# Kernel tuning notes

Measured on AMD Instinct MI355X. Metric: run time of the kernel, lower is better.

## Reference

```python
import jax, jax.numpy as jnp
import numpy as np

B, D, A = 512, 32, 10
NUM_CODES, CODE_DIM = 512, 64
COMMIT = 0.25


def _conv(x, w, b):
    # NHWC input, HWIO kernel, SAME padding, stride 1 (flax nn.Conv defaults)
    y = jax.lax.conv_general_dilated(x, w, (1, 1), 'SAME',
                                     dimension_numbers=('NHWC', 'HWIO', 'NHWC'))
    return y + b


def setup_inputs() -> dict:
    key = jax.random.key(0)
    ks = jax.random.split(key, 16)
    def rn(k, shape, scale):
        return jax.random.normal(k, shape, dtype=jnp.float32) * scale
    inp = {
        'x': rn(ks[0], (B, D, D), 1.0),
        'conv1_w': rn(ks[1], (3, 3, 1, 32), 0.3),
        'conv1_b': jnp.zeros((32,), jnp.float32),
        'conv2_w': rn(ks[2], (3, 3, 32, 64), 0.06),
        'conv2_b': jnp.zeros((64,), jnp.float32),
        'codebook': rn(ks[3], (NUM_CODES, CODE_DIM), 0.12),  # variance_scaling fan_in-ish
        'w1': rn(ks[4], (D * D * 64, 128), 0.004),
        'b1': jnp.zeros((128,), jnp.float32),
        'w2': rn(ks[5], (128, 128), 0.09),
        'b2': jnp.zeros((128,), jnp.float32),
        'w3': rn(ks[6], (128, 128), 0.09),
        'b3': jnp.zeros((128,), jnp.float32),
        'wa1': rn(ks[7], (128, 128), 0.09),
        'ba1': jnp.zeros((128,), jnp.float32),
        'wa2': rn(ks[8], (128, A), 0.09),
        'ba2': jnp.zeros((A,), jnp.float32),
        'wc1': rn(ks[9], (128, 128), 0.09),
        'bc1': jnp.zeros((128,), jnp.float32),
        'wc2': rn(ks[10], (128, 128), 0.09),
        'bc2': jnp.zeros((128,), jnp.float32),
        'wc3': rn(ks[11], (128, 1), 0.09),
        'bc3': jnp.zeros((1,), jnp.float32),
    }
    return inp


def reference(x, conv1_w, conv1_b, conv2_w, conv2_b, codebook,
              w1, b1, w2, b2, w3, b3,
              wa1, ba1, wa2, ba2,
              wc1, bc1, wc2, bc2, wc3, bc3):
    h = x.reshape(-1, D, D, 1)
    h = jax.nn.relu(_conv(h, conv1_w, conv1_b))
    h = jax.nn.relu(_conv(h, conv2_w, conv2_b))  # [B, D, D, 64]

    # --- Vector quantization (cdist + argmin + gather, straight-through) ---
    flat = h.reshape(-1, CODE_DIM)  # [B*D*D, 64]
    distances = (jnp.sum(flat ** 2, axis=1, keepdims=True)
                 - 2.0 * flat @ codebook.T
                 + jnp.sum(codebook ** 2, axis=1)[None, :])  # [N, num_codes]
    encoding_indices = jnp.argmin(distances, axis=1)
    quantized = codebook[encoding_indices].reshape(h.shape)
    quantized = h + jax.lax.stop_gradient(quantized - h)  # straight-through
    e_latent = jnp.mean((jax.lax.stop_gradient(quantized) - h) ** 2)
    q_latent = jnp.mean((quantized - jax.lax.stop_gradient(h)) ** 2)
    vq_loss = q_latent + COMMIT * e_latent

    # --- MLP trunk + actor-critic heads ---
    emb = quantized.reshape(quantized.shape[0], -1)
    emb = jax.nn.relu(emb @ w1 + b1)
    emb = jax.nn.relu(emb @ w2 + b2)
    emb = jax.nn.relu(emb @ w3 + b3)

    a = jax.nn.relu(emb @ wa1 + ba1)
    probs = jax.nn.softmax(a @ wa2 + ba2, axis=-1)  # Categorical probs

    c = jax.nn.relu(emb @ wc1 + bc1)
    c = jax.nn.relu(c @ wc2 + bc2)
    value = jnp.squeeze(c @ wc3 + bc3, axis=-1)

    return probs, value, vq_loss, encoding_indices
```

## Files before the change

### kernel.cpp

```cpp
#include <hip/hip_runtime.h>
#include <math.h>

#define NB 512
#define DD 32
#define NPX 1024
#define NTOT 524288
#define NC 512
#define CD 64

typedef float v2f __attribute__((ext_vector_type(2)));
typedef _Float16 hf;
typedef hf hf8 __attribute__((ext_vector_type(8)));
typedef float f32x4 __attribute__((ext_vector_type(4)));

__device__ __forceinline__ v2f pkfma(v2f a, v2f b, v2f c) {
    return __builtin_elementwise_fma(a, b, c);
}
__device__ __forceinline__ v2f splat2(float s) { v2f r; r.x = s; r.y = s; return r; }

__device__ __forceinline__ f32x4 mfma16(hf8 a, hf8 b, f32x4 c) {
    return __builtin_amdgcn_mfma_f32_16x16x32_f16(a, b, c, 0, 0, 0);
}

__device__ __forceinline__ float np_sumsq64(const float* a, int stride) {
    float r[8];
    #pragma unroll
    for (int j = 0; j < 8; ++j) {
        float v = a[j * stride];
        r[j] = __fmul_rn(v, v);
    }
    #pragma unroll
    for (int i = 1; i < 8; ++i)
        #pragma unroll
        for (int j = 0; j < 8; ++j) {
            float v = a[(i * 8 + j) * stride];
            r[j] = __fadd_rn(r[j], __fmul_rn(v, v));
        }
    return __fadd_rn(__fadd_rn(__fadd_rn(r[0], r[1]), __fadd_rn(r[2], r[3])),
                     __fadd_rn(__fadd_rn(r[4], r[5]), __fadd_rn(r[6], r[7])));
}

__global__ __launch_bounds__(256) void k_conv1(const float* __restrict__ x,
                                               const float* __restrict__ w,
                                               const float* __restrict__ bias,
                                               float* __restrict__ h1,
                                               const float* __restrict__ cb,
                                               const float* __restrict__ c2w,
                                               float* __restrict__ cnorm,
                                               hf* __restrict__ cbh,
                                               hf* __restrict__ cbl,
                                               hf* __restrict__ wTh,
                                               hf* __restrict__ wTl,
                                               float* __restrict__ accv) {
    const int b = blockIdx.x;
    const int tid = threadIdx.x;
    {
        int t = b * 256 + tid;
        if (t < NC)
            cnorm[t] = np_sumsq64(cb + (size_t)t * CD, 1);
        if (b < 128) {
            float a = cb[t] * 256.f;
            hf h0 = (hf)a;
            float rl = (a - (float)h0) * 2048.f;
            cbh[t] = h0;
            cbl[t] = (hf)rl;
        }
        if (b >= 128 && b < 200) {
            int t2 = (b - 128) * 256 + tid;
            if (t2 < 18432) {
                int s9 = t2 >> 11, rem = t2 & 2047;
                int co = rem >> 5, ci = rem & 31;
                float a = c2w[s9 * 2048 + ci * 64 + co] * 256.f;
                hf h0 = (hf)a;
                float rl = (a - (float)h0) * 2048.f;
                wTh[t2] = h0;
                wTl[t2] = (hf)rl;
            }
        }
        if (t == 0) accv[0] = 0.f;
    }
    __shared__ float xs[34][34];
    for (int i = tid; i < 34 * 34; i += 256) {
        int yy = i / 34, xx = i - yy * 34;
        float v = 0.f;
        if (yy >= 1 && yy <= 32 && xx >= 1 && xx <= 32)
            v = x[(size_t)b * NPX + (yy - 1) * 32 + (xx - 1)];
        xs[yy][xx] = v;
    }
    __syncthreads();
    for (int rep = 0; rep < 4; ++rep) {
        int px = tid + rep * 256;
        int y = px >> 5, xc = px & 31;
        v2f acc2[16];
        #pragma unroll
        for (int c = 0; c < 16; ++c) acc2[c] = splat2(0.f);
        #pragma unroll
        for (int dy = 0; dy < 3; ++dy)
        #pragma unroll
        for (int dx = 0; dx < 3; ++dx) {
            float a = xs[y + dy][xc + dx];
            v2f av = splat2(a);
            const v2f* wr = (const v2f*)(w + (dy * 3 + dx) * 32);
            #pragma unroll
            for (int c = 0; c < 16; ++c) acc2[c] = pkfma(av, wr[c], acc2[c]);
        }
        float4* out = (float4*)(h1 + ((size_t)b * NPX + px) * 32);
        #pragma unroll
        for (int q = 0; q < 8; ++q) {
            float4 v;
            v.x = fmaxf(__fadd_rn(acc2[q*2+0].x, bias[q*4+0]), 0.f);
            v.y = fmaxf(__fadd_rn(acc2[q*2+0].y, bias[q*4+1]), 0.f);
            v.z = fmaxf(__fadd_rn(acc2[q*2+1].x, bias[q*4+2]), 0.f);
            v.w = fmaxf(__fadd_rn(acc2[q*2+1].y, bias[q*4+3]), 0.f);
            out[q] = v;
        }
    }
}

#define CI_P 40
__global__ __launch_bounds__(512, 4) void k_conv2(const float* __restrict__ h1,
                                                  const hf* __restrict__ wTh,
                                                  const hf* __restrict__ wTl,
                                                  const float* __restrict__ bias,
                                                  float* __restrict__ h) {
    __shared__ hf Ah[10 * 34 * CI_P];
    __shared__ hf Al[10 * 34 * CI_P];
    const int blk = blockIdx.x;
    const int b = blk >> 2, strip = blk & 3;
    const int r0 = strip * 8;
    const int tid = threadIdx.x;
    for (int i = tid; i < 640; i += 512) {
        int ci = i & 31, rem = i >> 5;
        int ry = rem >> 1, colx = (rem & 1) * 33;
        int idx = (ry * 34 + colx) * CI_P + ci;
        Ah[idx] = (hf)0.f;
        Al[idx] = (hf)0.f;
    }
    #pragma unroll
    for (int r = 0; r < 5; ++r) {
        int j = tid + r * 512;
        int ci4 = j & 7, xc = (j >> 3) & 31, ry = j >> 8;
        int gy = r0 - 1 + ry;
        float4 v = make_float4(0.f, 0.f, 0.f, 0.f);
        if (gy >= 0 && gy < 32)
            v = *(const float4*)(h1 + ((size_t)b * NPX + gy * 32 + xc) * 32 + ci4 * 4);
        int bi = (ry * 34 + xc + 1) * CI_P + ci4 * 4;
        float fv[4] = {v.x, v.y, v.z, v.w};
        #pragma unroll
        for (int q = 0; q < 4; ++q) {
            float a = fv[q] * 256.f;
            hf h0 = (hf)a;
            float rl = (a - (float)h0) * 2048.f;
            Ah[bi + q] = h0;
            Al[bi + q] = (hf)rl;
        }
    }
    __syncthreads();
    const int w = tid >> 6, l = tid & 63;
    const int i16 = l & 15, j4 = l >> 4;
    #pragma unroll 1
    for (int ntp = 0; ntp < 2; ++ntp) {
        f32x4 hi[2][2], mid[2][2], llt[2][2];
        #pragma unroll
        for (int s = 0; s < 2; ++s)
            #pragma unroll
            for (int n = 0; n < 2; ++n) {
                hi[s][n] = f32x4{0.f, 0.f, 0.f, 0.f};
                mid[s][n] = f32x4{0.f, 0.f, 0.f, 0.f};
                llt[s][n] = f32x4{0.f, 0.f, 0.f, 0.f};
            }
        #pragma unroll 1
        for (int s9 = 0; s9 < 9; ++s9) {
            const int dy = s9 / 3, dx = s9 - dy * 3;
            hf8 a_h[2], a_l[2];
            #pragma unroll
            for (int s = 0; s < 2; ++s) {
                int ofs = ((w + dy) * 34 + (s * 16 + i16 + dx)) * CI_P + 8 * j4;
                a_h[s] = *(const hf8*)(Ah + ofs);
                a_l[s] = *(const hf8*)(Al + ofs);
            }
            #pragma unroll
            for (int ntl = 0; ntl < 2; ++ntl) {
                const int nt = ntp * 2 + ntl;
                const int wofs = (s9 * 64 + nt * 16 + i16) * 32 + 8 * j4;
                const hf8 b_h = *(const hf8*)(wTh + wofs);
                const hf8 b_l = *(const hf8*)(wTl + wofs);
                #pragma unroll
                for (int s = 0; s < 2; ++s) {
                    hi[s][ntl]  = mfma16(a_h[s], b_h, hi[s][ntl]);
                    mid[s][ntl] = mfma16(a_h[s], b_l, mid[s][ntl]);
                    mid[s][ntl] = mfma16(a_l[s], b_h, mid[s][ntl]);
                    llt[s][ntl] = mfma16(a_l[s], b_l, llt[s][ntl]);
                }
            }
        }
        #pragma unroll
        for (int ntl = 0; ntl < 2; ++ntl) {
            const int co = (ntp * 2 + ntl) * 16 + i16;
            const float bco = bias[co];
            #pragma unroll
            for (int s = 0; s < 2; ++s) {
                #pragma unroll
                for (int r = 0; r < 4; ++r) {
                    float comb = fmaf(mid[s][ntl][r], 4.8828125e-4f,
                                 fmaf(llt[s][ntl][r], 2.384185791015625e-7f,
                                      hi[s][ntl][r]));
                    float hv = fmaxf(
                        __fadd_rn(__fmul_rn(comb, 1.52587890625e-5f), bco), 0.f);
                    int px = w * 32 + s * 16 + j4 * 4 + r;
                    h[((size_t)b * NPX + r0 * 32 + px) * 64 + co] = hv;
                }
            }
        }
    }
}

#define TAU 1e-3f
__global__ __launch_bounds__(512, 4) void k_vq(const float* __restrict__ h,
                                               const float* __restrict__ h1,
                                               const float* __restrict__ c2w,
                                               const float* __restrict__ c2b,
                                               const float* __restrict__ cb,
                                               const hf* __restrict__ cbh,
                                               const hf* __restrict__ cbl,
                                               const float* __restrict__ cnorm,
                                               int* __restrict__ idxout,
                                               float* __restrict__ fidx,
                                               float* __restrict__ lossacc) {
    __shared__ float4 Ats[16][256];
    __shared__ float Hs[256];
    __shared__ float cn_lds[512];
    __shared__ int   mis_lds[256];
    __shared__ float r_v[512];
    __shared__ int   r_i[512];
    __shared__ int   rlist[256];
    __shared__ float hex_lds[64];
    __shared__ int   rcnt;
    const int tid = threadIdx.x;
    const size_t base = (size_t)blockIdx.x * 256;
    if (tid == 0) rcnt = 0;
    {
        const int px = tid & 255, half = tid >> 8;
        const float4* src = (const float4*)(h + (base + px) * 64 + half * 32);
        #pragma unroll
        for (int j = 0; j < 8; ++j)
            Ats[half * 8 + j][px] = src[j];
    }
    cn_lds[tid] = cnorm[tid];
    __syncthreads();
    if (tid < 256) {
        float f[64];
        #pragma unroll
        for (int kg = 0; kg < 16; ++kg) {
            float4 v = Ats[kg][tid];
            f[kg*4+0] = v.x; f[kg*4+1] = v.y; f[kg*4+2] = v.z; f[kg*4+3] = v.w;
        }
        float r[8];
        #pragma unroll
        for (int j = 0; j < 8; ++j) r[j] = __fmul_rn(f[j], f[j]);
        #pragma unroll
        for (int i = 1; i < 8; ++i)
            #pragma unroll
            for (int j = 0; j < 8; ++j)
                r[j] = __fadd_rn(r[j], __fmul_rn(f[i*8+j], f[i*8+j]));
        Hs[tid] = __fadd_rn(__fadd_rn(__fadd_rn(r[0], r[1]), __fadd_rn(r[2], r[3])),
                            __fadd_rn(__fadd_rn(r[4], r[5]), __fadd_rn(r[6], r[7])));
    }
    __syncthreads();
    const int w = tid >> 6, l = tid & 63;
    const int co = l & 15, g = l >> 4;
    const int pxw = w * 32;
    hf8 ah[2][2], al[2][2];
    #pragma unroll
    for (int s = 0; s < 2; ++s)
        #pragma unroll
        for (int ks = 0; ks < 2; ++ks) {
            float4 q0 = Ats[ks * 8 + g * 2 + 0][pxw + s * 16 + co];
            float4 q1 = Ats[ks * 8 + g * 2 + 1][pxw + s * 16 + co];
            float fv[8] = {q0.x, q0.y, q0.z, q0.w, q1.x, q1.y, q1.z, q1.w};
            #pragma unroll
            for (int j = 0; j < 8; ++j) {
                float fa = fv[j] * 256.f;
                hf h0 = (hf)fa;
                float rl = (fa - (float)h0) * 2048.f;
                ah[s][ks][j] = h0;
                al[s][ks][j] = (hf)rl;
            }
        }
    float Hr[2][4];
    #pragma unroll
    for (int s = 0; s < 2; ++s)
        #pragma unroll
        for (int r = 0; r < 4; ++r)
            Hr[s][r] = Hs[pxw + s * 16 + g * 4 + r];
    float minv[2][4], min2[2][4];
    int   mini[2][4];
    #pragma unroll
    for (int s = 0; s < 2; ++s)
        #pragma unroll
        for (int r = 0; r < 4; ++r) {
            minv[s][r] = 3.4e38f; min2[s][r] = 3.4e38f; mini[s][r] = 0;
        }
    const hf* pbh = cbh + (size_t)co * 64 + g * 8;
    const hf* pbl = cbl + (size_t)co * 64 + g * 8;
    #pragma unroll 1
    for (int t = 0; t < 32; ++t) {
        const hf8 bh0 = *(const hf8*)(pbh + (size_t)t * 1024);
        const hf8 bh1 = *(const hf8*)(pbh + (size_t)t * 1024 + 32);
        const hf8 bl0 = *(const hf8*)(pbl + (size_t)t * 1024);
        const hf8 bl1 = *(const hf8*)(pbl + (size_t)t * 1024 + 32);
        const float cn = cn_lds[t * 16 + co];
        #pragma unroll
        for (int s = 0; s < 2; ++s) {
            f32x4 hi = {0.f, 0.f, 0.f, 0.f};
            f32x4 lo = {0.f, 0.f, 0.f, 0.f};
            f32x4 ll = {0.f, 0.f, 0.f, 0.f};
            lo = mfma16(ah[s][0], bl0, lo);
            lo = mfma16(al[s][0], bh0, lo);
            ll = mfma16(al[s][0], bl0, ll);
            hi = mfma16(ah[s][0], bh0, hi);
            lo = mfma16(ah[s][1], bl1, lo);
            lo = mfma16(al[s][1], bh1, lo);
            ll = mfma16(al[s][1], bl1, ll);
            hi = mfma16(ah[s][1], bh1, hi);
            #pragma unroll
            for (int r = 0; r < 4; ++r) {
                float comb = fmaf(lo[r], 4.8828125e-4f,
                             fmaf(ll[r], 2.384185791015625e-7f, hi[r]));
                float d = __fadd_rn(__fsub_rn(Hr[s][r],
                              __fmul_rn(3.0517578125e-5f, comb)), cn);
                if (d < minv[s][r]) {
                    min2[s][r] = minv[s][r];
                    minv[s][r] = d; mini[s][r] = t * 16 + co;
                } else if (d < min2[s][r]) {
                    min2[s][r] = d;
                }
            }
        }
    }
    #pragma unroll
    for (int s = 0; s < 2; ++s)
        #pragma unroll
        for (int r = 0; r < 4; ++r) {
            float v1 = minv[s][r], v2 = min2[s][r];
            int i1 = mini[s][r];
            #pragma unroll
            for (int off = 1; off < 16; off <<= 1) {
                float vo  = __shfl_xor(v1, off, 64);
                int   io  = __shfl_xor(i1, off, 64);
                float v2o = __shfl_xor(v2, off, 64);
                if (vo < v1 || (vo == v1 && io < i1)) {
                    v2 = fminf(v1, v2o);
                    v1 = vo; i1 = io;
                } else {
                    v2 = fminf(v2, vo);
                }
            }
            if (co == 0) {
                int pxo = pxw + s * 16 + g * 4 + r;
                mis_lds[pxo] = i1;
                if (v2 - v1 <= TAU) {
                    int slot = atomicAdd(&rcnt, 1);
                    rlist[slot] = pxo;
                }
            }
        }
    __syncthreads();
    const int nresc = rcnt;
    for (int rr = 0; rr < nresc; ++rr) {
        const int px = rlist[rr];
        const int gpx = (int)base + px;
        const int bimg = gpx >> 10, pp = gpx & 1023;
        const int py = pp >> 5, pxx = pp & 31;
        if (tid < 64) {
            float acc = 0.f;
            #pragma unroll 1
            for (int s9 = 0; s9 < 9; ++s9) {
                const int dy = s9 / 3, dx = s9 - dy * 3;
                const int gy = py + dy - 1, gx = pxx + dx - 1;
                if (gy >= 0 && gy < 32 && gx >= 0 && gx < 32) {
                    const float* hp = h1 + ((size_t)bimg * NPX + gy * 32 + gx) * 32;
                    const float* wp = c2w + s9 * 2048 + tid;
                    #pragma unroll
                    for (int ci = 0; ci < 32; ++ci)
                        acc = fmaf(hp[ci], wp[ci * 64], acc);
                }
            }
            hex_lds[tid] = fmaxf(__fadd_rn(acc, c2b[tid]), 0.f);
        }
        __syncthreads();
        const float Hp = np_sumsq64(hex_lds, 1);
        float acc0 = 0.f;
        const float* crow0 = cb + (size_t)tid * 64;
        #pragma unroll
        for (int kg = 0; kg < 16; ++kg) {
            acc0 = fmaf(hex_lds[kg*4+0], crow0[kg*4+0], acc0);
            acc0 = fmaf(hex_lds[kg*4+1], crow0[kg*4+1], acc0);
            acc0 = fmaf(hex_lds[kg*4+2], crow0[kg*4+2], acc0);
            acc0 = fmaf(hex_lds[kg*4+3], crow0[kg*4+3], acc0);
        }
        r_v[tid] = __fadd_rn(__fsub_rn(Hp, __fmul_rn(2.f, acc0)), cn_lds[tid]);
        r_i[tid] = tid;
        __syncthreads();
        for (int st = 256; st > 0; st >>= 1) {
            if (tid < st) {
                float vo = r_v[tid + st]; int io = r_i[tid + st];
                if (vo < r_v[tid] || (vo == r_v[tid] && io < r_i[tid])) {
                    r_v[tid] = vo; r_i[tid] = io;
                }
            }
            __syncthreads();
        }
        if (tid == 0) mis_lds[px] = r_i[0];
        __syncthreads();
    }
    if (tid < 256) {
        int bi = mis_lds[tid];
        idxout[base + tid] = bi;
        fidx[base + tid] = (float)bi;
        float ls = 0.f;
        const float* crow = cb + (size_t)bi * 64;
        #pragma unroll
        for (int kg = 0; kg < 16; ++kg) {
            float4 a = Ats[kg][tid];
            float d0 = crow[kg*4+0] - a.x;
            float d1 = crow[kg*4+1] - a.y;
            float d2 = crow[kg*4+2] - a.z;
            float d3 = crow[kg*4+3] - a.w;
            ls = fmaf(d0, d0, ls); ls = fmaf(d1, d1, ls);
            ls = fmaf(d2, d2, ls); ls = fmaf(d3, d3, ls);
        }
        #pragma unroll
        for (int off = 32; off > 0; off >>= 1)
            ls += __shfl_down(ls, off, 64);
        if ((tid & 63) == 0) atomicAdd(lossacc, ls);
    }
}

__global__ __launch_bounds__(256) void k_prepw1(const float* __restrict__ w1,
                                                hf* __restrict__ w1h,
                                                hf* __restrict__ w1l) {
    int t = blockIdx.x * 256 + threadIdx.x;
    int n = t & 127, k8 = t >> 7;
    hf vh[8], vl[8];
    #pragma unroll
    for (int j = 0; j < 8; ++j) {
        float a = w1[(size_t)(k8 * 8 + j) * 128 + n] * 256.f;
        hf h0 = (hf)a;
        float rl = (a - (float)h0) * 2048.f;
        vh[j] = h0;
        vl[j] = (hf)rl;
    }
    *(hf8*)(w1h + (size_t)k8 * 1024 + n * 8) = *(hf8*)vh;
    *(hf8*)(w1l + (size_t)k8 * 1024 + n * 8) = *(hf8*)vl;
}

__global__ __launch_bounds__(256) void k_fc1(const int* __restrict__ idxw,
                                             const hf* __restrict__ cbh,
                                             const hf* __restrict__ cbl,
                                             const hf* __restrict__ w1h,
                                             const hf* __restrict__ w1l,
                                             float* __restrict__ part) {
    const int kchunk = blockIdx.x;
    const int mtile  = blockIdx.y;
    const int tid = threadIdx.x;
    const int w = tid >> 6, l = tid & 63;
    const int co = l & 15, g = l >> 4;
    const int mbase = mtile * 64 + w * 16;
    f32x4 hi[8], mid[8];
    #pragma unroll
    for (int n = 0; n < 8; ++n) {
        hi[n] = f32x4{0.f, 0.f, 0.f, 0.f};
        mid[n] = f32x4{0.f, 0.f, 0.f, 0.f};
    }
    int code = 0;
    #pragma unroll 1
    for (int kstep = 0; kstep < 32; ++kstep) {
        if ((kstep & 1) == 0) {
            const int pix = kchunk * 16 + (kstep >> 1);
            code = idxw[(size_t)(mbase + co) * NPX + pix];
        }
        const int koff = (kstep & 1) * 32 + g * 8;
        const hf8 ah = *(const hf8*)(cbh + ((size_t)code << 6) + koff);
        const hf8 al = *(const hf8*)(cbl + ((size_t)code << 6) + koff);
        const size_t k8b = (size_t)(kchunk * 128 + kstep * 4 + g) * 1024;
        #pragma unroll
        for (int n = 0; n < 8; ++n) {
            const hf8 bh = *(const hf8*)(w1h + k8b + (n * 16 + co) * 8);
            const hf8 bl = *(const hf8*)(w1l + k8b + (n * 16 + co) * 8);
            hi[n]  = mfma16(ah, bh, hi[n]);
            mid[n] = mfma16(ah, bl, mid[n]);
            mid[n] = mfma16(al, bh, mid[n]);
        }
    }
    #pragma unroll
    for (int n = 0; n < 8; ++n)
        #pragma unroll
        for (int r = 0; r < 4; ++r) {
            float comb = fmaf(mid[n][r], 4.8828125e-4f, hi[n][r]);
            const int img = mtile * 64 + w * 16 + g * 4 + r;
            part[((size_t)kchunk * 512 + img) * 128 + n * 16 + co] =
                __fmul_rn(comb, 1.52587890625e-5f);
        }
}

__global__ __launch_bounds__(256) void k_reduce(const float* __restrict__ part,
                                                const float* __restrict__ b1,
                                                float* __restrict__ x0) {
    int t = blockIdx.x * 256 + threadIdx.x;
    float s = b1[t & 127];
    for (int ch = 0; ch < 64; ++ch)
        s += part[(size_t)ch * 65536 + t];
    x0[t] = fmaxf(s, 0.f);
}

__device__ __forceinline__ void mlp_layer(const float in[][16], float out[][16],
                                          const float* __restrict__ W,
                                          const float* __restrict__ bias,
                                          int tid, bool dorelu) {
    const int lane = tid & 63, wv = tid >> 6;
    const int img = lane & 15, cg = lane >> 4;
    const int c0 = wv * 32 + cg * 8;
    float acc[8] = {0,0,0,0,0,0,0,0};
    for (int k = 0; k < 128; ++k) {
        float a = in[k][img];
        float4 wA = *(const float4*)(W + (size_t)k * 128 + c0);
        float4 wB = *(const float4*)(W + (size_t)k * 128 + c0 + 4);
        acc[0] = fmaf(a, wA.x, acc[0]);
        acc[1] = fmaf(a, wA.y, acc[1]);
        acc[2] = fmaf(a, wA.z, acc[2]);
        acc[3] = fmaf(a, wA.w, acc[3]);
        acc[4] = fmaf(a, wB.x, acc[4]);
        acc[5] = fmaf(a, wB.y, acc[5]);
        acc[6] = fmaf(a, wB.z, acc[6]);
        acc[7] = fmaf(a, wB.w, acc[7]);
    }
    #pragma unroll
    for (int c = 0; c < 8; ++c) {
        float v = acc[c] + bias[c0 + c];
        if (dorelu) v = fmaxf(v, 0.f);
        out[c0 + c][img] = v;
    }
}

__global__ __launch_bounds__(256) void k_trunk(const float* __restrict__ x0,
        const float* __restrict__ w2, const float* __restrict__ b2,
        const float* __restrict__ w3, const float* __restrict__ b3,
        const float* __restrict__ wa1, const float* __restrict__ ba1,
        const float* __restrict__ wa2, const float* __restrict__ ba2,
        const float* __restrict__ wc1, const float* __restrict__ bc1,
        const float* __restrict__ wc2, const float* __restrict__ bc2,
        const float* __restrict__ wc3, const float* __restrict__ bc3,
        float* __restrict__ probs, float* __restrict__ value,
        const float* __restrict__ accv, float* __restrict__ vqloss) {
    __shared__ float bufA[128][16], bufB[128][16], bufC[128][16];
    __shared__ float lg[16][10];
    const int tid = threadIdx.x;
    const int m0 = blockIdx.x * 16;
    if (blockIdx.x == 0 && tid == 0)
        vqloss[0] = accv[0] * 1.25f / 33554432.f;
    for (int r = 0; r < 2; ++r) {
        int j = tid + r * 256;
        int img = j >> 5, k4 = j & 31;
        float4 v = *(const float4*)(x0 + (size_t)(m0 + img) * 128 + k4 * 4);
        bufA[k4*4+0][img] = v.x;
        bufA[k4*4+1][img] = v.y;
        bufA[k4*4+2][img] = v.z;
        bufA[k4*4+3][img] = v.w;
    }
    __syncthreads();
    mlp_layer(bufA, bufB, w2, b2, tid, true);   __syncthreads();
    mlp_layer(bufB, bufC, w3, b3, tid, true);   __syncthreads();
    mlp_layer(bufC, bufA, wa1, ba1, tid, true); __syncthreads();
    if (tid < 160) {
        int img = tid & 15, col = tid >> 4;
        float s = 0.f;
        for (int k = 0; k < 128; ++k)
            s = fmaf(bufA[k][img], wa2[(size_t)k * 10 + col], s);
        lg[img][col] = s + ba2[col];
    }
    __syncthreads();
    if (tid < 16) {
        int img = tid;
        float m = lg[img][0];
        #pragma unroll
        for (int c = 1; c < 10; ++c) m = fmaxf(m, lg[img][c]);
        float e[10]; float s = 0.f;
        #pragma unroll
        for (int c = 0; c < 10; ++c) { e[c] = expf(lg[img][c] - m); s += e[c]; }
        float inv = 1.f / s;
        #pragma unroll
        for (int c = 0; c < 10; ++c)
            probs[(size_t)(m0 + img) * 10 + c] = e[c] * inv;
    }
    __syncthreads();
    mlp_layer(bufC, bufB, wc1, bc1, tid, true); __syncthreads();
    mlp_layer(bufB, bufA, wc2, bc2, tid, true); __syncthreads();
    if (tid < 16) {
        int img = tid;
        float s = 0.f;
        for (int k = 0; k < 128; ++k)
            s = fmaf(bufA[k][img], wc3[k], s);
        value[m0 + img] = s + bc3[0];
    }
}

extern "C" void kernel_launch(void* const* d_in, const int* in_sizes, int n_in,
                              void* d_out, int out_size, void* d_ws, size_t ws_size,
                              hipStream_t stream) {
    const float* x   = (const float*)d_in[0];
    const float* c1w = (const float*)d_in[1];
    const float* c1b = (const float*)d_in[2];
    const float* c2w = (const float*)d_in[3];
    const float* c2b = (const float*)d_in[4];
    const float* cb  = (const float*)d_in[5];
    const float* w1  = (const float*)d_in[6];
    const float* b1  = (const float*)d_in[7];
    const float* w2  = (const float*)d_in[8];
    const float* b2  = (const float*)d_in[9];
    const float* w3  = (const float*)d_in[10];
    const float* b3  = (const float*)d_in[11];
    const float* wa1 = (const float*)d_in[12];
    const float* ba1 = (const float*)d_in[13];
    const float* wa2 = (const float*)d_in[14];
    const float* ba2 = (const float*)d_in[15];
    const float* wc1 = (const float*)d_in[16];
    const float* bc1 = (const float*)d_in[17];
    const float* wc2 = (const float*)d_in[18];
    const float* bc2 = (const float*)d_in[19];
    const float* wc3 = (const float*)d_in[20];
    const float* bc3 = (const float*)d_in[21];

    float* out = (float*)d_out;
    float* ws  = (float*)d_ws;

    float* h1    = ws;
    float* part  = ws;
    float* x0    = ws + (size_t)4 * 1024 * 1024;
    float* h     = ws + (size_t)16 * 1024 * 1024;
    hf*    w1Th  = (hf*)(ws + (size_t)16777216);
    hf*    w1Tl  = (hf*)(ws + (size_t)20971520);
    int*   idxw  = (int*)(ws + (size_t)50331648);
    float* cn    = ws + (size_t)50855936;
    float* accv  = ws + (size_t)50856448;
    hf*    cbh   = (hf*)(ws + (size_t)50857984);
    hf*    cbl   = (hf*)(ws + (size_t)50874368);
    hf*    wTh   = (hf*)(ws + (size_t)50890752);
    hf*    wTl   = (hf*)(ws + (size_t)50899968);

    hipLaunchKernelGGL(k_conv1,  dim3(512),   dim3(256), 0, stream, x, c1w, c1b, h1,
                       cb, c2w, cn, cbh, cbl, wTh, wTl, accv);
    hipLaunchKernelGGL(k_conv2,  dim3(2048),  dim3(512), 0, stream, h1, wTh, wTl,
                       c2b, h);
    hipLaunchKernelGGL(k_vq,     dim3(2048),  dim3(512), 0, stream, h, h1, c2w, c2b,
                       cb, cbh, cbl, cn, idxw, out + 5633, accv);
    hipLaunchKernelGGL(k_prepw1, dim3(4096),  dim3(256), 0, stream, w1, w1Th, w1Tl);
    hipLaunchKernelGGL(k_fc1,    dim3(64, 8), dim3(256), 0, stream, idxw, cbh, cbl,
                       w1Th, w1Tl, part);
    hipLaunchKernelGGL(k_reduce, dim3(256),   dim3(256), 0, stream, part, b1, x0);
    hipLaunchKernelGGL(k_trunk,  dim3(32),    dim3(256), 0, stream, x0,
                       w2, b2, w3, b3, wa1, ba1, wa2, ba2,
                       wc1, bc1, wc2, bc2, wc3, bc3,
                       out, out + 5120, accv, out + 5632);
}
```

Before: 736.0 us.

## Drop row norm and lo*lo MFMA from VQ distances, prefetch codebook tiles

```diff
diff --git a/kernel.cpp b/kernel.cpp
--- a/kernel.cpp
+++ b/kernel.cpp
@@ -228,7 +228,6 @@
                                                float* __restrict__ fidx,
                                                float* __restrict__ lossacc) {
     __shared__ float4 Ats[16][256];
-    __shared__ float Hs[256];
     __shared__ float cn_lds[512];
     __shared__ int   mis_lds[256];
     __shared__ float r_v[512];
@@ -248,25 +247,6 @@
     }
     cn_lds[tid] = cnorm[tid];
     __syncthreads();
-    if (tid < 256) {
-        float f[64];
-        #pragma unroll
-        for (int kg = 0; kg < 16; ++kg) {
-            float4 v = Ats[kg][tid];
-            f[kg*4+0] = v.x; f[kg*4+1] = v.y; f[kg*4+2] = v.z; f[kg*4+3] = v.w;
-        }
-        float r[8];
-        #pragma unroll
-        for (int j = 0; j < 8; ++j) r[j] = __fmul_rn(f[j], f[j]);
-        #pragma unroll
-        for (int i = 1; i < 8; ++i)
-            #pragma unroll
-            for (int j = 0; j < 8; ++j)
-                r[j] = __fadd_rn(r[j], __fmul_rn(f[i*8+j], f[i*8+j]));
-        Hs[tid] = __fadd_rn(__fadd_rn(__fadd_rn(r[0], r[1]), __fadd_rn(r[2], r[3])),
-                            __fadd_rn(__fadd_rn(r[4], r[5]), __fadd_rn(r[6], r[7])));
-    }
-    __syncthreads();
     const int w = tid >> 6, l = tid & 63;
     const int co = l & 15, g = l >> 4;
     const int pxw = w * 32;
@@ -287,12 +267,6 @@
                 al[s][ks][j] = (hf)rl;
             }
         }
-    float Hr[2][4];
-    #pragma unroll
-    for (int s = 0; s < 2; ++s)
-        #pragma unroll
-        for (int r = 0; r < 4; ++r)
-            Hr[s][r] = Hs[pxw + s * 16 + g * 4 + r];
     float minv[2][4], min2[2][4];
     int   mini[2][4];
     #pragma unroll
@@ -303,32 +277,32 @@
         }
     const hf* pbh = cbh + (size_t)co * 64 + g * 8;
     const hf* pbl = cbl + (size_t)co * 64 + g * 8;
+    hf8 Ch0 = *(const hf8*)(pbh);
+    hf8 Ch1 = *(const hf8*)(pbh + 32);
+    hf8 Cl0 = *(const hf8*)(pbl);
+    hf8 Cl1 = *(const hf8*)(pbl + 32);
     #pragma unroll 1
     for (int t = 0; t < 32; ++t) {
-        const hf8 bh0 = *(const hf8*)(pbh + (size_t)t * 1024);
-        const hf8 bh1 = *(const hf8*)(pbh + (size_t)t * 1024 + 32);
-        const hf8 bl0 = *(const hf8*)(pbl + (size_t)t * 1024);
-        const hf8 bl1 = *(const hf8*)(pbl + (size_t)t * 1024 + 32);
+        const int tn = (t + 1 < 32) ? t + 1 : 31;
+        hf8 Nh0 = *(const hf8*)(pbh + (size_t)tn * 1024);
+        hf8 Nh1 = *(const hf8*)(pbh + (size_t)tn * 1024 + 32);
+        hf8 Nl0 = *(const hf8*)(pbl + (size_t)tn * 1024);
+        hf8 Nl1 = *(const hf8*)(pbl + (size_t)tn * 1024 + 32);
         const float cn = cn_lds[t * 16 + co];
         #pragma unroll
         for (int s = 0; s < 2; ++s) {
             f32x4 hi = {0.f, 0.f, 0.f, 0.f};
             f32x4 lo = {0.f, 0.f, 0.f, 0.f};
-            f32x4 ll = {0.f, 0.f, 0.f, 0.f};
-            lo = mfma16(ah[s][0], bl0, lo);
-            lo = mfma16(al[s][0], bh0, lo);
-            ll = mfma16(al[s][0], bl0, ll);
-            hi = mfma16(ah[s][0], bh0, hi);
-            lo = mfma16(ah[s][1], bl1, lo);
-            lo = mfma16(al[s][1], bh1, lo);
-            ll = mfma16(al[s][1], bl1, ll);
-            hi = mfma16(ah[s][1], bh1, hi);
+            lo = mfma16(ah[s][0], Cl0, lo);
+            lo = mfma16(al[s][0], Ch0, lo);
+            hi = mfma16(ah[s][0], Ch0, hi);
+            lo = mfma16(ah[s][1], Cl1, lo);
+            lo = mfma16(al[s][1], Ch1, lo);
+            hi = mfma16(ah[s][1], Ch1, hi);
             #pragma unroll
             for (int r = 0; r < 4; ++r) {
-                float comb = fmaf(lo[r], 4.8828125e-4f,
-                             fmaf(ll[r], 2.384185791015625e-7f, hi[r]));
-                float d = __fadd_rn(__fsub_rn(Hr[s][r],
-                              __fmul_rn(3.0517578125e-5f, comb)), cn);
+                float comb = fmaf(lo[r], 4.8828125e-4f, hi[r]);
+                float d = __fsub_rn(cn, __fmul_rn(3.0517578125e-5f, comb));
                 if (d < minv[s][r]) {
                     min2[s][r] = minv[s][r];
                     minv[s][r] = d; mini[s][r] = t * 16 + co;
@@ -337,6 +311,7 @@
                 }
             }
         }
+        Ch0 = Nh0; Ch1 = Nh1; Cl0 = Nl0; Cl1 = Nl1;
     }
     #pragma unroll
     for (int s = 0; s < 2; ++s)
```

Result: no change. 741.5 us (+0.8%).

## Parallelize VQ rescue across waves and drop constant row-norm term

Applied to the files above, without the earlier changes.

```diff
diff --git a/kernel.cpp b/kernel.cpp
--- a/kernel.cpp
+++ b/kernel.cpp
@@ -215,7 +215,7 @@
     }
 }
 
-#define TAU 1e-3f
+#define TAU 2e-4f
 __global__ __launch_bounds__(512, 4) void k_vq(const float* __restrict__ h,
                                                const float* __restrict__ h1,
                                                const float* __restrict__ c2w,
@@ -228,13 +228,10 @@
                                                float* __restrict__ fidx,
                                                float* __restrict__ lossacc) {
     __shared__ float4 Ats[16][256];
-    __shared__ float Hs[256];
     __shared__ float cn_lds[512];
     __shared__ int   mis_lds[256];
-    __shared__ float r_v[512];
-    __shared__ int   r_i[512];
     __shared__ int   rlist[256];
-    __shared__ float hex_lds[64];
+    __shared__ float hex[8][64];
     __shared__ int   rcnt;
     const int tid = threadIdx.x;
     const size_t base = (size_t)blockIdx.x * 256;
@@ -248,25 +245,6 @@
     }
     cn_lds[tid] = cnorm[tid];
     __syncthreads();
-    if (tid < 256) {
-        float f[64];
-        #pragma unroll
-        for (int kg = 0; kg < 16; ++kg) {
-            float4 v = Ats[kg][tid];
-            f[kg*4+0] = v.x; f[kg*4+1] = v.y; f[kg*4+2] = v.z; f[kg*4+3] = v.w;
-        }
-        float r[8];
-        #pragma unroll
-        for (int j = 0; j < 8; ++j) r[j] = __fmul_rn(f[j], f[j]);
-        #pragma unroll
-        for (int i = 1; i < 8; ++i)
-            #pragma unroll
-            for (int j = 0; j < 8; ++j)
-                r[j] = __fadd_rn(r[j], __fmul_rn(f[i*8+j], f[i*8+j]));
-        Hs[tid] = __fadd_rn(__fadd_rn(__fadd_rn(r[0], r[1]), __fadd_rn(r[2], r[3])),
-                            __fadd_rn(__fadd_rn(r[4], r[5]), __fadd_rn(r[6], r[7])));
-    }
-    __syncthreads();
     const int w = tid >> 6, l = tid & 63;
     const int co = l & 15, g = l >> 4;
     const int pxw = w * 32;
@@ -287,12 +265,6 @@
                 al[s][ks][j] = (hf)rl;
             }
         }
-    float Hr[2][4];
-    #pragma unroll
-    for (int s = 0; s < 2; ++s)
-        #pragma unroll
-        for (int r = 0; r < 4; ++r)
-            Hr[s][r] = Hs[pxw + s * 16 + g * 4 + r];
     float minv[2][4], min2[2][4];
     int   mini[2][4];
     #pragma unroll
@@ -327,8 +299,7 @@
             for (int r = 0; r < 4; ++r) {
                 float comb = fmaf(lo[r], 4.8828125e-4f,
                              fmaf(ll[r], 2.384185791015625e-7f, hi[r]));
-                float d = __fadd_rn(__fsub_rn(Hr[s][r],
-                              __fmul_rn(3.0517578125e-5f, comb)), cn);
+                float d = __fsub_rn(cn, __fmul_rn(3.0517578125e-5f, comb));
                 if (d < minv[s][r]) {
                     min2[s][r] = minv[s][r];
                     minv[s][r] = d; mini[s][r] = t * 16 + co;
@@ -367,12 +338,13 @@
         }
     __syncthreads();
     const int nresc = rcnt;
-    for (int rr = 0; rr < nresc; ++rr) {
+    for (int rr = w; rr < nresc; rr += 8) {
         const int px = rlist[rr];
         const int gpx = (int)base + px;
         const int bimg = gpx >> 10, pp = gpx & 1023;
         const int py = pp >> 5, pxx = pp & 31;
-        if (tid < 64) {
+        float* hx = &hex[w][0];
+        {
             float acc = 0.f;
             #pragma unroll 1
             for (int s9 = 0; s9 < 9; ++s9) {
@@ -380,40 +352,41 @@
                 const int gy = py + dy - 1, gx = pxx + dx - 1;
                 if (gy >= 0 && gy < 32 && gx >= 0 && gx < 32) {
                     const float* hp = h1 + ((size_t)bimg * NPX + gy * 32 + gx) * 32;
-                    const float* wp = c2w + s9 * 2048 + tid;
+                    const float* wp = c2w + s9 * 2048 + l;
                     #pragma unroll
                     for (int ci = 0; ci < 32; ++ci)
                         acc = fmaf(hp[ci], wp[ci * 64], acc);
                 }
             }
-            hex_lds[tid] = fmaxf(__fadd_rn(acc, c2b[tid]), 0.f);
-        }
-        __syncthreads();
-        const float Hp = np_sumsq64(hex_lds, 1);
-        float acc0 = 0.f;
-        const float* crow0 = cb + (size_t)tid * 64;
-        #pragma unroll
-        for (int kg = 0; kg < 16; ++kg) {
-            acc0 = fmaf(hex_lds[kg*4+0], crow0[kg*4+0], acc0);
-            acc0 = fmaf(hex_lds[kg*4+1], crow0[kg*4+1], acc0);
-            acc0 = fmaf(hex_lds[kg*4+2], crow0[kg*4+2], acc0);
-            acc0 = fmaf(hex_lds[kg*4+3], crow0[kg*4+3], acc0);
-        }
-        r_v[tid] = __fadd_rn(__fsub_rn(Hp, __fmul_rn(2.f, acc0)), cn_lds[tid]);
-        r_i[tid] = tid;
-        __syncthreads();
-        for (int st = 256; st > 0; st >>= 1) {
-            if (tid < st) {
-                float vo = r_v[tid + st]; int io = r_i[tid + st];
-                if (vo < r_v[tid] || (vo == r_v[tid] && io < r_i[tid])) {
-                    r_v[tid] = vo; r_i[tid] = io;
-                }
-            }
-            __syncthreads();
-        }
-        if (tid == 0) mis_lds[px] = r_i[0];
-        __syncthreads();
-    }
+            hx[l] = fmaxf(__fadd_rn(acc, c2b[l]), 0.f);
+        }
+        const float Hp = np_sumsq64(hx, 1);
+        float bv = 3.4e38f; int bi2 = 0;
+        const float* crow = cb + (size_t)(l * 8) * 64;
+        #pragma unroll 1
+        for (int c = 0; c < 8; ++c) {
+            float acc0 = 0.f;
+            const float* cr = crow + c * 64;
+            #pragma unroll
+            for (int kg = 0; kg < 16; ++kg) {
+                acc0 = fmaf(hx[kg*4+0], cr[kg*4+0], acc0);
+                acc0 = fmaf(hx[kg*4+1], cr[kg*4+1], acc0);
+                acc0 = fmaf(hx[kg*4+2], cr[kg*4+2], acc0);
+                acc0 = fmaf(hx[kg*4+3], cr[kg*4+3], acc0);
+            }
+            float d = __fadd_rn(__fsub_rn(Hp, __fmul_rn(2.f, acc0)),
+                                cn_lds[l * 8 + c]);
+            if (d < bv) { bv = d; bi2 = l * 8 + c; }
+        }
+        #pragma unroll
+        for (int off = 1; off < 64; off <<= 1) {
+            float vo = __shfl_xor(bv, off, 64);
+            int   io = __shfl_xor(bi2, off, 64);
+            if (vo < bv || (vo == bv && io < bi2)) { bv = vo; bi2 = io; }
+        }
+        if (l == 0) mis_lds[px] = bi2;
+    }
+    __syncthreads();
     if (tid < 256) {
         int bi = mis_lds[tid];
         idxout[base + tid] = bi;
```

After: 710.7 us. 1.04x faster.
